# Performance work log

Hardware: AMD Instinct MI355X
Metric: run time of the kernel (lower is better)

The kernel has to match this reference:

```python
import jax, jax.numpy as jnp
import numpy as np

N = 100000
E = 1600000
F_IN = 4
HID = 8
HEADS = 8
NEG_SLOPE = 0.2


def setup_inputs() -> dict:
    key = jax.random.key(0)
    ks = jax.random.split(key, 12)
    x = jax.random.normal(ks[0], (N, F_IN), dtype=jnp.float32)
    edge_index = jax.random.randint(ks[1], (2, E), 0, N, dtype=jnp.int64)
    s = 0.3
    W1 = jax.random.normal(ks[2], (F_IN, HEADS * HID), dtype=jnp.float32) * s
    att_src1 = jax.random.normal(ks[3], (HEADS, HID), dtype=jnp.float32) * s
    att_dst1 = jax.random.normal(ks[4], (HEADS, HID), dtype=jnp.float32) * s
    b1 = jnp.zeros((HEADS * HID,), dtype=jnp.float32)
    W2 = jax.random.normal(ks[5], (HEADS * HID, 1), dtype=jnp.float32) * s
    att_src2 = jax.random.normal(ks[6], (1, 1), dtype=jnp.float32) * s
    att_dst2 = jax.random.normal(ks[7], (1, 1), dtype=jnp.float32) * s
    b2 = jnp.zeros((1,), dtype=jnp.float32)
    return {"x": x, "edge_index": edge_index, "W1": W1, "att_src1": att_src1,
            "att_dst1": att_dst1, "b1": b1, "W2": W2, "att_src2": att_src2,
            "att_dst2": att_dst2, "b2": b2}


def gat_conv(x, src, dst, W, att_s, att_d, b, heads, out_ch, concat):
    n = x.shape[0]
    h = (x @ W).reshape(n, heads, out_ch)              # [N,H,C]
    a_s = jnp.sum(h * att_s, axis=-1)                  # [N,H]
    a_d = jnp.sum(h * att_d, axis=-1)                  # [N,H]
    e = jax.nn.leaky_relu(a_s[src] + a_d[dst], NEG_SLOPE)  # [E,H]
    # segment softmax over edges grouped by destination node
    m = jax.ops.segment_max(e, dst, num_segments=n)
    e = jnp.exp(e - m[dst])
    denom = jax.ops.segment_sum(e, dst, num_segments=n)
    alpha = e / (denom[dst] + 1e-16)                   # [E,H]
    msg = h[src] * alpha[..., None]                    # [E,H,C]
    out = jax.ops.segment_sum(msg, dst, num_segments=n)  # [N,H,C]
    out = out.reshape(n, heads * out_ch) if concat else out.mean(axis=1)
    return out + b


def reference(x, edge_index, W1, att_src1, att_dst1, b1, W2, att_src2, att_dst2, b2):
    n = x.shape[0]
    loops = jnp.arange(n, dtype=edge_index.dtype)
    src = jnp.concatenate([edge_index[0], loops])
    dst = jnp.concatenate([edge_index[1], loops])
    h = gat_conv(x, src, dst, W1, att_src1, att_dst1, b1, HEADS, HID, True)
    h = jax.nn.elu(h)
    out = gat_conv(h, src, dst, W2, att_src2, att_dst2, b2, 1, 1, False)
    return jax.nn.sigmoid(out)
```

## Files before the change

### kernel.cpp

```cpp
#include <hip/hip_runtime.h>

#define NN 100000
#define NE 1600000
#define NBKT 391
#define CAP 8192
#define TILE 4096
#define NTILE ((NE + TILE - 1) / TILE)
#define NEG 0.2f

__global__ __launch_bounds__(512) void kU_prep(
    const float* __restrict__ W1, const float* __restrict__ atts,
    const float* __restrict__ attd, float* __restrict__ us, float* __restrict__ ud,
    int* __restrict__ bcnt)
{
    int t = threadIdx.x;
    if (t < NBKT) bcnt[t] = 0;
    if (t < 64) {
        int half = t >> 5;
        int i = t & 31;
        int h = i >> 2, k = i & 3;
        const float* att = half ? attd : atts;
        float acc = 0.f;
        #pragma unroll
        for (int j = 0; j < 8; j++)
            acc += W1[k * 64 + h * 8 + j] * att[h * 8 + j];
        (half ? ud : us)[h * 4 + k] = acc;
    }
}

__global__ __launch_bounds__(1024) void kP1_tile(
    const int* __restrict__ ei, int* __restrict__ bcnt, unsigned* __restrict__ bpack)
{
    __shared__ unsigned sarr[TILE];
    __shared__ int lh[512], lsc[512], lgb[512];
    int t = threadIdx.x;
    int e0 = blockIdx.x * TILE;
    int n = NE - e0; if (n > TILE) n = TILE;

    if (t < 512) lh[t] = 0;
    __syncthreads();
    for (int i = t; i < n; i += 1024) {
        int d = ei[NE + e0 + i];
        atomicAdd(&lh[d >> 8], 1);
    }
    __syncthreads();
    if (t < 512) lsc[t] = lh[t];
    __syncthreads();
    #pragma unroll
    for (int o = 1; o < 512; o <<= 1) {
        int u = 0;
        if (t < 512 && t >= o) u = lsc[t - o];
        __syncthreads();
        if (t < 512) lsc[t] += u;
        __syncthreads();
    }
    if (t < NBKT && lh[t] > 0) lgb[t] = atomicAdd(&bcnt[t], lh[t]);
    __syncthreads();
    if (t < 512) lh[t] = lsc[t] - lh[t];
    __syncthreads();
    for (int i = t; i < n; i += 1024) {
        int s = ei[e0 + i], d = ei[NE + e0 + i];
        int b = d >> 8;
        int pos = atomicAdd(&lh[b], 1);
        sarr[pos] = ((unsigned)s << 8) | (unsigned)(d & 255);
    }
    __syncthreads();
    int wave = t >> 6, lane = t & 63;
    for (int b = wave; b < NBKT; b += 16) {
        int start = (b == 0) ? 0 : lsc[b - 1];
        int cntb = lsc[b] - start;
        if (cntb == 0) continue;
        int gb = lgb[b];
        unsigned* dstp = &bpack[(size_t)b * CAP];
        for (int j = lane; j < cntb; j += 64) {
            int gpos = gb + j;
            if (gpos < CAP) dstp[gpos] = sarr[start + j];
        }
    }
}

__global__ __launch_bounds__(512) void kS_scan(
    const int* __restrict__ bcnt, int* __restrict__ bktoff, int* __restrict__ row)
{
    __shared__ int s[512];
    int t = threadIdx.x;
    int v = (t < NBKT) ? bcnt[t] : 0;
    s[t] = v;
    __syncthreads();
    #pragma unroll
    for (int o = 1; o < 512; o <<= 1) {
        int u = (t >= o) ? s[t - o] : 0;
        __syncthreads();
        s[t] += u;
        __syncthreads();
    }
    if (t < NBKT) bktoff[t] = s[t] - v;
    if (t == 0) row[NN] = NE;
}

__global__ __launch_bounds__(1024) void kP2_build(
    const int* __restrict__ bcnt, const int* __restrict__ bktoff,
    const unsigned* __restrict__ bpack, int* __restrict__ row, int* __restrict__ esrc)
{
    __shared__ int lh[256], lsc[256], lcur[256];
    __shared__ int sarr[CAP];
    int b = blockIdx.x;
    int t = threadIdx.x;
    int cnt = bcnt[b];
    if (cnt > CAP) cnt = CAP;
    const unsigned* bp = &bpack[(size_t)b * CAP];
    if (t < 256) lh[t] = 0;
    __syncthreads();
    for (int i = t; i < cnt; i += 1024)
        atomicAdd(&lh[bp[i] & 255u], 1);
    __syncthreads();
    if (t < 256) lsc[t] = lh[t];
    __syncthreads();
    #pragma unroll
    for (int o = 1; o < 256; o <<= 1) {
        int u = 0;
        if (t < 256 && t >= o) u = lsc[t - o];
        __syncthreads();
        if (t < 256) lsc[t] += u;
        __syncthreads();
    }
    int base = bktoff[b];
    if (t < 256) {
        int ex = lsc[t] - lh[t];
        lcur[t] = ex;
        int node = b * 256 + t;
        if (node < NN) row[node] = base + ex;
    }
    __syncthreads();
    for (int i = t; i < cnt; i += 1024) {
        unsigned u = bp[i];
        int pos = atomicAdd(&lcur[u & 255u], 1);
        sarr[pos] = (int)(u >> 8);
    }
    __syncthreads();
    for (int i = t; i < cnt; i += 1024)
        esrc[base + i] = sarr[i];
}

__global__ __launch_bounds__(256) void kE_l1agg(
    const int* __restrict__ row, const int* __restrict__ esrc,
    const float* __restrict__ x, const float* __restrict__ us,
    const float* __restrict__ ud, const float* __restrict__ W1,
    const float* __restrict__ b1, const float* __restrict__ W2,
    float* __restrict__ h2)
{
    int t = threadIdx.x;
    int grp = t >> 3;
    int h   = t & 7;
    int dst = blockIdx.x * 32 + grp;
    if (dst >= NN) return;

    int start = row[dst], end = row[dst + 1];
    int m = end - start;

    float4 u  = *reinterpret_cast<const float4*>(&us[h * 4]);
    float4 vd = *reinterpret_cast<const float4*>(&ud[h * 4]);
    float4 xd = *reinterpret_cast<const float4*>(&x[(size_t)dst * 4]);
    float adj = xd.x * vd.x + xd.y * vd.y + xd.z * vd.z + xd.w * vd.w;

    float a0 = fmaf(xd.x, u.x, fmaf(xd.y, u.y, fmaf(xd.z, u.z, fmaf(xd.w, u.w, adj))));
    a0 = fmaxf(a0, NEG * a0);
    float p0 = __expf(a0);
    float den = p0;
    float xa0 = p0 * xd.x, xa1 = p0 * xd.y, xa2 = p0 * xd.z, xa3 = p0 * xd.w;

    int j = 0;
    for (; j + 2 <= m; j += 2) {
        int s0 = esrc[start + j];
        int s1 = esrc[start + j + 1];
        float4 q0 = *reinterpret_cast<const float4*>(&x[(size_t)s0 * 4]);
        float4 q1 = *reinterpret_cast<const float4*>(&x[(size_t)s1 * 4]);
        float b0 = fmaf(q0.x, u.x, fmaf(q0.y, u.y, fmaf(q0.z, u.z, fmaf(q0.w, u.w, adj))));
        float c1 = fmaf(q1.x, u.x, fmaf(q1.y, u.y, fmaf(q1.z, u.z, fmaf(q1.w, u.w, adj))));
        b0 = fmaxf(b0, NEG * b0);
        c1 = fmaxf(c1, NEG * c1);
        float pb = __expf(b0);
        float pc = __expf(c1);
        den += pb + pc;
        xa0 = fmaf(pb, q0.x, fmaf(pc, q1.x, xa0));
        xa1 = fmaf(pb, q0.y, fmaf(pc, q1.y, xa1));
        xa2 = fmaf(pb, q0.z, fmaf(pc, q1.z, xa2));
        xa3 = fmaf(pb, q0.w, fmaf(pc, q1.w, xa3));
    }
    if (j < m) {
        int s0 = esrc[start + j];
        float4 q0 = *reinterpret_cast<const float4*>(&x[(size_t)s0 * 4]);
        float b0 = fmaf(q0.x, u.x, fmaf(q0.y, u.y, fmaf(q0.z, u.z, fmaf(q0.w, u.w, adj))));
        b0 = fmaxf(b0, NEG * b0);
        float pb = __expf(b0);
        den += pb;
        xa0 = fmaf(pb, q0.x, xa0);
        xa1 = fmaf(pb, q0.y, xa1);
        xa2 = fmaf(pb, q0.z, xa2);
        xa3 = fmaf(pb, q0.w, xa3);
    }

    int c0 = h * 8;
    float4 w0l = *reinterpret_cast<const float4*>(&W1[c0]);
    float4 w0h = *reinterpret_cast<const float4*>(&W1[c0 + 4]);
    float4 w1l = *reinterpret_cast<const float4*>(&W1[64 + c0]);
    float4 w1h = *reinterpret_cast<const float4*>(&W1[64 + c0 + 4]);
    float4 w2l = *reinterpret_cast<const float4*>(&W1[128 + c0]);
    float4 w2h = *reinterpret_cast<const float4*>(&W1[128 + c0 + 4]);
    float4 w3l = *reinterpret_cast<const float4*>(&W1[192 + c0]);
    float4 w3h = *reinterpret_cast<const float4*>(&W1[192 + c0 + 4]);
    float4 bbl = *reinterpret_cast<const float4*>(&b1[c0]);
    float4 bbh = *reinterpret_cast<const float4*>(&b1[c0 + 4]);
    float4 wwl = *reinterpret_cast<const float4*>(&W2[c0]);
    float4 wwh = *reinterpret_cast<const float4*>(&W2[c0 + 4]);
    float inv = 1.f / (den + 1e-16f);

    float acc = 0.f;
    {
        float v;
        v = (xa0*w0l.x + xa1*w1l.x + xa2*w2l.x + xa3*w3l.x)*inv + bbl.x;
        v = v > 0.f ? v : (__expf(v) - 1.f);  acc += v * wwl.x;
        v = (xa0*w0l.y + xa1*w1l.y + xa2*w2l.y + xa3*w3l.y)*inv + bbl.y;
        v = v > 0.f ? v : (__expf(v) - 1.f);  acc += v * wwl.y;
        v = (xa0*w0l.z + xa1*w1l.z + xa2*w2l.z + xa3*w3l.z)*inv + bbl.z;
        v = v > 0.f ? v : (__expf(v) - 1.f);  acc += v * wwl.z;
        v = (xa0*w0l.w + xa1*w1l.w + xa2*w2l.w + xa3*w3l.w)*inv + bbl.w;
        v = v > 0.f ? v : (__expf(v) - 1.f);  acc += v * wwl.w;
        v = (xa0*w0h.x + xa1*w1h.x + xa2*w2h.x + xa3*w3h.x)*inv + bbh.x;
        v = v > 0.f ? v : (__expf(v) - 1.f);  acc += v * wwh.x;
        v = (xa0*w0h.y + xa1*w1h.y + xa2*w2h.y + xa3*w3h.y)*inv + bbh.y;
        v = v > 0.f ? v : (__expf(v) - 1.f);  acc += v * wwh.y;
        v = (xa0*w0h.z + xa1*w1h.z + xa2*w2h.z + xa3*w3h.z)*inv + bbh.z;
        v = v > 0.f ? v : (__expf(v) - 1.f);  acc += v * wwh.z;
        v = (xa0*w0h.w + xa1*w1h.w + xa2*w2h.w + xa3*w3h.w)*inv + bbh.w;
        v = v > 0.f ? v : (__expf(v) - 1.f);  acc += v * wwh.w;
    }
    acc += __shfl_xor(acc, 1, 8);
    acc += __shfl_xor(acc, 2, 8);
    acc += __shfl_xor(acc, 4, 8);
    if (h == 0) h2[dst] = acc;
}

__global__ __launch_bounds__(256) void kF_l2agg(
    const int* __restrict__ row, const int* __restrict__ esrc,
    const float* __restrict__ h2, const float* __restrict__ as2,
    const float* __restrict__ ad2, const float* __restrict__ b2,
    float* __restrict__ out)
{
    int t = threadIdx.x;
    int grp = t >> 3;
    int sub = t & 7;
    int dst = blockIdx.x * 32 + grp;
    if (dst >= NN) return;
    int start = row[dst], end = row[dst + 1];
    float a_s = as2[0], a_d = ad2[0];
    float hdv = h2[dst];
    float hd = hdv * a_d;

    float den = 0.f, num = 0.f;
    if (sub == 0) {
        float v = hdv * a_s + hd;
        v = fmaxf(v, NEG * v);
        float p = __expf(v);
        den = p;
        num = p * hdv;
    }
    int i = start + sub;
    for (; i + 8 < end; i += 16) {
        float hs0 = h2[esrc[i]];
        float hs1 = h2[esrc[i + 8]];
        float v0 = hs0 * a_s + hd;
        float v1 = hs1 * a_s + hd;
        v0 = fmaxf(v0, NEG * v0);
        v1 = fmaxf(v1, NEG * v1);
        float p0 = __expf(v0);
        float p1 = __expf(v1);
        den += p0 + p1;
        num = fmaf(p0, hs0, fmaf(p1, hs1, num));
    }
    if (i < end) {
        float hs = h2[esrc[i]];
        float v = hs * a_s + hd;
        v = fmaxf(v, NEG * v);
        float p = __expf(v);
        den += p;
        num = fmaf(p, hs, num);
    }
    den += __shfl_xor(den, 1, 8);
    num += __shfl_xor(num, 1, 8);
    den += __shfl_xor(den, 2, 8);
    num += __shfl_xor(num, 2, 8);
    den += __shfl_xor(den, 4, 8);
    num += __shfl_xor(num, 4, 8);
    if (sub == 0) {
        float v = num / (den + 1e-16f) + b2[0];
        out[dst] = 1.f / (1.f + __expf(-v));
    }
}

extern "C" void kernel_launch(void* const* d_in, const int* in_sizes, int n_in,
                              void* d_out, int out_size, void* d_ws, size_t ws_size,
                              hipStream_t stream) {
    const float* x     = (const float*)d_in[0];
    const int*   ei    = (const int*)d_in[1];
    const float* W1    = (const float*)d_in[2];
    const float* atts1 = (const float*)d_in[3];
    const float* attd1 = (const float*)d_in[4];
    const float* b1    = (const float*)d_in[5];
    const float* W2    = (const float*)d_in[6];
    const float* atts2 = (const float*)d_in[7];
    const float* attd2 = (const float*)d_in[8];
    const float* b2    = (const float*)d_in[9];
    float* out = (float*)d_out;

    float* w = (float*)d_ws;
    float* us = w;
    float* ud = w + 32;
    float* h2 = w + 64;
    int* ibase  = (int*)(w + 64 + (size_t)NN);
    int* bcnt   = ibase;
    int* bktoff = ibase + 512;
    int* row    = ibase + 1024;
    int* esrc   = ibase + 1024 + NN + 64;
    unsigned* bpack = (unsigned*)(ibase + 1024 + NN + 64 + NE);

    dim3 gG((NN + 31) / 32);

    hipLaunchKernelGGL(kU_prep, dim3(1), dim3(512), 0, stream, W1, atts1, attd1, us, ud, bcnt);
    hipLaunchKernelGGL(kP1_tile, dim3(NTILE), dim3(1024), 0, stream, ei, bcnt, bpack);
    hipLaunchKernelGGL(kS_scan, dim3(1), dim3(512), 0, stream, bcnt, bktoff, row);
    hipLaunchKernelGGL(kP2_build, dim3(NBKT), dim3(1024), 0, stream, bcnt, bktoff, bpack, row, esrc);
    hipLaunchKernelGGL(kE_l1agg, gG, dim3(256), 0, stream, row, esrc, x, us, ud, W1, b1, W2, h2);
    hipLaunchKernelGGL(kF_l2agg, gG, dim3(256), 0, stream, row, esrc, h2, atts2, attd2, b2, out);
}
```

Measured before the change: 75.58 us.

## Fuse CSR build into per-bucket layer-1 aggregation and drop global scan

Removes the global bucket-offset scan and the CSR materialization (row/esrc). The per-bucket local sort now runs inside the layer-1 aggregation kernel, with neighbor lists kept in shared memory. Layer 2 aggregates straight from the unsorted bucket pack using shared-memory float atomics. This cuts two launches and the global esrc write and read, at the cost of 391-block grids, lower parallelism per node, and truncation at LCAP=6144 edges per bucket.

```diff
diff --git a/kernel.cpp b/kernel.cpp
--- a/kernel.cpp
+++ b/kernel.cpp
@@ -4,6 +4,7 @@
 #define NE 1600000
 #define NBKT 391
 #define CAP 8192
+#define LCAP 6144
 #define TILE 4096
 #define NTILE ((NE + TILE - 1) / TILE)
 #define NEG 0.2f
@@ -79,36 +80,22 @@
     }
 }
 
-__global__ __launch_bounds__(512) void kS_scan(
-    const int* __restrict__ bcnt, int* __restrict__ bktoff, int* __restrict__ row)
-{
-    __shared__ int s[512];
-    int t = threadIdx.x;
-    int v = (t < NBKT) ? bcnt[t] : 0;
-    s[t] = v;
-    __syncthreads();
-    #pragma unroll
-    for (int o = 1; o < 512; o <<= 1) {
-        int u = (t >= o) ? s[t - o] : 0;
-        __syncthreads();
-        s[t] += u;
-        __syncthreads();
-    }
-    if (t < NBKT) bktoff[t] = s[t] - v;
-    if (t == 0) row[NN] = NE;
-}
-
-__global__ __launch_bounds__(1024) void kP2_build(
-    const int* __restrict__ bcnt, const int* __restrict__ bktoff,
-    const unsigned* __restrict__ bpack, int* __restrict__ row, int* __restrict__ esrc)
+__global__ __launch_bounds__(1024) void kE_fused(
+    const int* __restrict__ bcnt, const unsigned* __restrict__ bpack,
+    const float* __restrict__ x, const float* __restrict__ us,
+    const float* __restrict__ ud, const float* __restrict__ W1,
+    const float* __restrict__ b1, const float* __restrict__ W2,
+    float* __restrict__ h2)
 {
     __shared__ int lh[256], lsc[256], lcur[256];
-    __shared__ int sarr[CAP];
-    int b = blockIdx.x;
-    int t = threadIdx.x;
-    int cnt = bcnt[b];
-    if (cnt > CAP) cnt = CAP;
+    __shared__ int sdat[LCAP];
+    __shared__ float sadj[256][8];
+    __shared__ float sxd[256][4];
+    int b = blockIdx.x, t = threadIdx.x;
+    int cnt = bcnt[b]; if (cnt > LCAP) cnt = LCAP;
     const unsigned* bp = &bpack[(size_t)b * CAP];
+    int node0 = b * 256;
+
     if (t < 256) lh[t] = 0;
     __syncthreads();
     for (int i = t; i < cnt; i += 1024)
@@ -124,82 +111,32 @@
         if (t < 256) lsc[t] += u;
         __syncthreads();
     }
-    int base = bktoff[b];
     if (t < 256) {
-        int ex = lsc[t] - lh[t];
-        lcur[t] = ex;
-        int node = b * 256 + t;
-        if (node < NN) row[node] = base + ex;
-    }
-    __syncthreads();
+        lcur[t] = lsc[t] - lh[t];
+        int node = node0 + t;
+        float4 xv = (node < NN) ? *reinterpret_cast<const float4*>(&x[(size_t)node * 4])
+                                : make_float4(0.f, 0.f, 0.f, 0.f);
+        sxd[t][0] = xv.x; sxd[t][1] = xv.y; sxd[t][2] = xv.z; sxd[t][3] = xv.w;
+    }
+    __syncthreads();
+    {
+        int dl = t >> 3, h = t & 7;
+        float4 vd = *reinterpret_cast<const float4*>(&ud[h * 4]);
+        #pragma unroll
+        for (int p = 0; p < 2; p++) {
+            int d = dl + 128 * p;
+            sadj[d][h] = sxd[d][0]*vd.x + sxd[d][1]*vd.y + sxd[d][2]*vd.z + sxd[d][3]*vd.w;
+        }
+    }
     for (int i = t; i < cnt; i += 1024) {
         unsigned u = bp[i];
         int pos = atomicAdd(&lcur[u & 255u], 1);
-        sarr[pos] = (int)(u >> 8);
-    }
-    __syncthreads();
-    for (int i = t; i < cnt; i += 1024)
-        esrc[base + i] = sarr[i];
-}
-
-__global__ __launch_bounds__(256) void kE_l1agg(
-    const int* __restrict__ row, const int* __restrict__ esrc,
-    const float* __restrict__ x, const float* __restrict__ us,
-    const float* __restrict__ ud, const float* __restrict__ W1,
-    const float* __restrict__ b1, const float* __restrict__ W2,
-    float* __restrict__ h2)
-{
-    int t = threadIdx.x;
-    int grp = t >> 3;
-    int h   = t & 7;
-    int dst = blockIdx.x * 32 + grp;
-    if (dst >= NN) return;
-
-    int start = row[dst], end = row[dst + 1];
-    int m = end - start;
-
-    float4 u  = *reinterpret_cast<const float4*>(&us[h * 4]);
-    float4 vd = *reinterpret_cast<const float4*>(&ud[h * 4]);
-    float4 xd = *reinterpret_cast<const float4*>(&x[(size_t)dst * 4]);
-    float adj = xd.x * vd.x + xd.y * vd.y + xd.z * vd.z + xd.w * vd.w;
-
-    float a0 = fmaf(xd.x, u.x, fmaf(xd.y, u.y, fmaf(xd.z, u.z, fmaf(xd.w, u.w, adj))));
-    a0 = fmaxf(a0, NEG * a0);
-    float p0 = __expf(a0);
-    float den = p0;
-    float xa0 = p0 * xd.x, xa1 = p0 * xd.y, xa2 = p0 * xd.z, xa3 = p0 * xd.w;
-
-    int j = 0;
-    for (; j + 2 <= m; j += 2) {
-        int s0 = esrc[start + j];
-        int s1 = esrc[start + j + 1];
-        float4 q0 = *reinterpret_cast<const float4*>(&x[(size_t)s0 * 4]);
-        float4 q1 = *reinterpret_cast<const float4*>(&x[(size_t)s1 * 4]);
-        float b0 = fmaf(q0.x, u.x, fmaf(q0.y, u.y, fmaf(q0.z, u.z, fmaf(q0.w, u.w, adj))));
-        float c1 = fmaf(q1.x, u.x, fmaf(q1.y, u.y, fmaf(q1.z, u.z, fmaf(q1.w, u.w, adj))));
-        b0 = fmaxf(b0, NEG * b0);
-        c1 = fmaxf(c1, NEG * c1);
-        float pb = __expf(b0);
-        float pc = __expf(c1);
-        den += pb + pc;
-        xa0 = fmaf(pb, q0.x, fmaf(pc, q1.x, xa0));
-        xa1 = fmaf(pb, q0.y, fmaf(pc, q1.y, xa1));
-        xa2 = fmaf(pb, q0.z, fmaf(pc, q1.z, xa2));
-        xa3 = fmaf(pb, q0.w, fmaf(pc, q1.w, xa3));
-    }
-    if (j < m) {
-        int s0 = esrc[start + j];
-        float4 q0 = *reinterpret_cast<const float4*>(&x[(size_t)s0 * 4]);
-        float b0 = fmaf(q0.x, u.x, fmaf(q0.y, u.y, fmaf(q0.z, u.z, fmaf(q0.w, u.w, adj))));
-        b0 = fmaxf(b0, NEG * b0);
-        float pb = __expf(b0);
-        den += pb;
-        xa0 = fmaf(pb, q0.x, xa0);
-        xa1 = fmaf(pb, q0.y, xa1);
-        xa2 = fmaf(pb, q0.z, xa2);
-        xa3 = fmaf(pb, q0.w, xa3);
-    }
-
+        sdat[pos] = (int)(u >> 8);
+    }
+    __syncthreads();
+
+    int h = t & 7;
+    float4 u4 = *reinterpret_cast<const float4*>(&us[h * 4]);
     int c0 = h * 8;
     float4 w0l = *reinterpret_cast<const float4*>(&W1[c0]);
     float4 w0h = *reinterpret_cast<const float4*>(&W1[c0 + 4]);
@@ -213,88 +150,119 @@
     float4 bbh = *reinterpret_cast<const float4*>(&b1[c0 + 4]);
     float4 wwl = *reinterpret_cast<const float4*>(&W2[c0]);
     float4 wwh = *reinterpret_cast<const float4*>(&W2[c0 + 4]);
-    float inv = 1.f / (den + 1e-16f);
-
-    float acc = 0.f;
-    {
-        float v;
-        v = (xa0*w0l.x + xa1*w1l.x + xa2*w2l.x + xa3*w3l.x)*inv + bbl.x;
-        v = v > 0.f ? v : (__expf(v) - 1.f);  acc += v * wwl.x;
-        v = (xa0*w0l.y + xa1*w1l.y + xa2*w2l.y + xa3*w3l.y)*inv + bbl.y;
-        v = v > 0.f ? v : (__expf(v) - 1.f);  acc += v * wwl.y;
-        v = (xa0*w0l.z + xa1*w1l.z + xa2*w2l.z + xa3*w3l.z)*inv + bbl.z;
-        v = v > 0.f ? v : (__expf(v) - 1.f);  acc += v * wwl.z;
-        v = (xa0*w0l.w + xa1*w1l.w + xa2*w2l.w + xa3*w3l.w)*inv + bbl.w;
-        v = v > 0.f ? v : (__expf(v) - 1.f);  acc += v * wwl.w;
-        v = (xa0*w0h.x + xa1*w1h.x + xa2*w2h.x + xa3*w3h.x)*inv + bbh.x;
-        v = v > 0.f ? v : (__expf(v) - 1.f);  acc += v * wwh.x;
-        v = (xa0*w0h.y + xa1*w1h.y + xa2*w2h.y + xa3*w3h.y)*inv + bbh.y;
-        v = v > 0.f ? v : (__expf(v) - 1.f);  acc += v * wwh.y;
-        v = (xa0*w0h.z + xa1*w1h.z + xa2*w2h.z + xa3*w3h.z)*inv + bbh.z;
-        v = v > 0.f ? v : (__expf(v) - 1.f);  acc += v * wwh.z;
-        v = (xa0*w0h.w + xa1*w1h.w + xa2*w2h.w + xa3*w3h.w)*inv + bbh.w;
-        v = v > 0.f ? v : (__expf(v) - 1.f);  acc += v * wwh.w;
-    }
-    acc += __shfl_xor(acc, 1, 8);
-    acc += __shfl_xor(acc, 2, 8);
-    acc += __shfl_xor(acc, 4, 8);
-    if (h == 0) h2[dst] = acc;
-}
-
-__global__ __launch_bounds__(256) void kF_l2agg(
-    const int* __restrict__ row, const int* __restrict__ esrc,
+
+    #pragma unroll
+    for (int p = 0; p < 2; p++) {
+        int dl = (t >> 3) + 128 * p;
+        int node = node0 + dl;
+        if (node < NN) {
+            int off = lsc[dl] - lh[dl];
+            int mdeg = lh[dl];
+            float adj = sadj[dl][h];
+            float xd0 = sxd[dl][0], xd1 = sxd[dl][1], xd2 = sxd[dl][2], xd3 = sxd[dl][3];
+            float a0 = fmaf(xd0, u4.x, fmaf(xd1, u4.y, fmaf(xd2, u4.z, fmaf(xd3, u4.w, adj))));
+            a0 = fmaxf(a0, NEG * a0);
+            float p0 = __expf(a0);
+            float den = p0;
+            float xa0 = p0 * xd0, xa1 = p0 * xd1, xa2 = p0 * xd2, xa3 = p0 * xd3;
+            int j = 0;
+            for (; j + 2 <= mdeg; j += 2) {
+                int s0 = sdat[off + j];
+                int s1 = sdat[off + j + 1];
+                float4 q0 = *reinterpret_cast<const float4*>(&x[(size_t)s0 * 4]);
+                float4 q1 = *reinterpret_cast<const float4*>(&x[(size_t)s1 * 4]);
+                float b0 = fmaf(q0.x, u4.x, fmaf(q0.y, u4.y, fmaf(q0.z, u4.z, fmaf(q0.w, u4.w, adj))));
+                float c1 = fmaf(q1.x, u4.x, fmaf(q1.y, u4.y, fmaf(q1.z, u4.z, fmaf(q1.w, u4.w, adj))));
+                b0 = fmaxf(b0, NEG * b0);
+                c1 = fmaxf(c1, NEG * c1);
+                float pb = __expf(b0);
+                float pc = __expf(c1);
+                den += pb + pc;
+                xa0 = fmaf(pb, q0.x, fmaf(pc, q1.x, xa0));
+                xa1 = fmaf(pb, q0.y, fmaf(pc, q1.y, xa1));
+                xa2 = fmaf(pb, q0.z, fmaf(pc, q1.z, xa2));
+                xa3 = fmaf(pb, q0.w, fmaf(pc, q1.w, xa3));
+            }
+            if (j < mdeg) {
+                int s0 = sdat[off + j];
+                float4 q0 = *reinterpret_cast<const float4*>(&x[(size_t)s0 * 4]);
+                float b0 = fmaf(q0.x, u4.x, fmaf(q0.y, u4.y, fmaf(q0.z, u4.z, fmaf(q0.w, u4.w, adj))));
+                b0 = fmaxf(b0, NEG * b0);
+                float pb = __expf(b0);
+                den += pb;
+                xa0 = fmaf(pb, q0.x, xa0);
+                xa1 = fmaf(pb, q0.y, xa1);
+                xa2 = fmaf(pb, q0.z, xa2);
+                xa3 = fmaf(pb, q0.w, xa3);
+            }
+            float inv = 1.f / (den + 1e-16f);
+            float acc = 0.f, v;
+            v = (xa0*w0l.x + xa1*w1l.x + xa2*w2l.x + xa3*w3l.x)*inv + bbl.x;
+            v = v > 0.f ? v : (__expf(v) - 1.f);  acc += v * wwl.x;
+            v = (xa0*w0l.y + xa1*w1l.y + xa2*w2l.y + xa3*w3l.y)*inv + bbl.y;
+            v = v > 0.f ? v : (__expf(v) - 1.f);  acc += v * wwl.y;
+            v = (xa0*w0l.z + xa1*w1l.z + xa2*w2l.z + xa3*w3l.z)*inv + bbl.z;
+            v = v > 0.f ? v : (__expf(v) - 1.f);  acc += v * wwl.z;
+            v = (xa0*w0l.w + xa1*w1l.w + xa2*w2l.w + xa3*w3l.w)*inv + bbl.w;
+            v = v > 0.f ? v : (__expf(v) - 1.f);  acc += v * wwl.w;
+            v = (xa0*w0h.x + xa1*w1h.x + xa2*w2h.x + xa3*w3h.x)*inv + bbh.x;
+            v = v > 0.f ? v : (__expf(v) - 1.f);  acc += v * wwh.x;
+            v = (xa0*w0h.y + xa1*w1h.y + xa2*w2h.y + xa3*w3h.y)*inv + bbh.y;
+            v = v > 0.f ? v : (__expf(v) - 1.f);  acc += v * wwh.y;
+            v = (xa0*w0h.z + xa1*w1h.z + xa2*w2h.z + xa3*w3h.z)*inv + bbh.z;
+            v = v > 0.f ? v : (__expf(v) - 1.f);  acc += v * wwh.z;
+            v = (xa0*w0h.w + xa1*w1h.w + xa2*w2h.w + xa3*w3h.w)*inv + bbh.w;
+            v = v > 0.f ? v : (__expf(v) - 1.f);  acc += v * wwh.w;
+            acc += __shfl_xor(acc, 1, 8);
+            acc += __shfl_xor(acc, 2, 8);
+            acc += __shfl_xor(acc, 4, 8);
+            if (h == 0) h2[node] = acc;
+        }
+    }
+}
+
+__global__ __launch_bounds__(1024) void kF_bucket(
+    const int* __restrict__ bcnt, const unsigned* __restrict__ bpack,
     const float* __restrict__ h2, const float* __restrict__ as2,
     const float* __restrict__ ad2, const float* __restrict__ b2,
     float* __restrict__ out)
 {
-    int t = threadIdx.x;
-    int grp = t >> 3;
-    int sub = t & 7;
-    int dst = blockIdx.x * 32 + grp;
-    if (dst >= NN) return;
-    int start = row[dst], end = row[dst + 1];
+    __shared__ float sh2[256], snum[256], sden[256];
+    int b = blockIdx.x, t = threadIdx.x;
+    int cnt = bcnt[b]; if (cnt > CAP) cnt = CAP;
+    const unsigned* bp = &bpack[(size_t)b * CAP];
     float a_s = as2[0], a_d = ad2[0];
-    float hdv = h2[dst];
-    float hd = hdv * a_d;
-
-    float den = 0.f, num = 0.f;
-    if (sub == 0) {
-        float v = hdv * a_s + hd;
+    if (t < 256) {
+        int node = b * 256 + t;
+        sh2[t] = (node < NN) ? h2[node] : 0.f;
+        snum[t] = 0.f;
+        sden[t] = 0.f;
+    }
+    __syncthreads();
+    for (int i = t; i < cnt; i += 1024) {
+        unsigned u = bp[i];
+        int s  = (int)(u >> 8);
+        int dl = (int)(u & 255u);
+        float hs = h2[s];
+        float v = fmaf(hs, a_s, sh2[dl] * a_d);
         v = fmaxf(v, NEG * v);
         float p = __expf(v);
-        den = p;
-        num = p * hdv;
-    }
-    int i = start + sub;
-    for (; i + 8 < end; i += 16) {
-        float hs0 = h2[esrc[i]];
-        float hs1 = h2[esrc[i + 8]];
-        float v0 = hs0 * a_s + hd;
-        float v1 = hs1 * a_s + hd;
-        v0 = fmaxf(v0, NEG * v0);
-        v1 = fmaxf(v1, NEG * v1);
-        float p0 = __expf(v0);
-        float p1 = __expf(v1);
-        den += p0 + p1;
-        num = fmaf(p0, hs0, fmaf(p1, hs1, num));
-    }
-    if (i < end) {
-        float hs = h2[esrc[i]];
-        float v = hs * a_s + hd;
-        v = fmaxf(v, NEG * v);
-        float p = __expf(v);
-        den += p;
-        num = fmaf(p, hs, num);
-    }
-    den += __shfl_xor(den, 1, 8);
-    num += __shfl_xor(num, 1, 8);
-    den += __shfl_xor(den, 2, 8);
-    num += __shfl_xor(num, 2, 8);
-    den += __shfl_xor(den, 4, 8);
-    num += __shfl_xor(num, 4, 8);
-    if (sub == 0) {
-        float v = num / (den + 1e-16f) + b2[0];
-        out[dst] = 1.f / (1.f + __expf(-v));
+        atomicAdd(&sden[dl], p);
+        atomicAdd(&snum[dl], p * hs);
+    }
+    __syncthreads();
+    if (t < 256) {
+        int node = b * 256 + t;
+        if (node < NN) {
+            float hdv = sh2[t];
+            float v = fmaf(hdv, a_s, hdv * a_d);
+            v = fmaxf(v, NEG * v);
+            float p0 = __expf(v);
+            float num = snum[t] + p0 * hdv;
+            float den = sden[t] + p0;
+            float r = num / (den + 1e-16f) + b2[0];
+            out[node] = 1.f / (1.f + __expf(-r));
+        }
     }
 }
 
@@ -317,19 +285,11 @@
     float* us = w;
     float* ud = w + 32;
     float* h2 = w + 64;
-    int* ibase  = (int*)(w + 64 + (size_t)NN);
-    int* bcnt   = ibase;
-    int* bktoff = ibase + 512;
-    int* row    = ibase + 1024;
-    int* esrc   = ibase + 1024 + NN + 64;
-    unsigned* bpack = (unsigned*)(ibase + 1024 + NN + 64 + NE);
-
-    dim3 gG((NN + 31) / 32);
+    int* bcnt = (int*)(w + 64 + (size_t)NN);
+    unsigned* bpack = (unsigned*)(w + 64 + (size_t)NN + 512);
 
     hipLaunchKernelGGL(kU_prep, dim3(1), dim3(512), 0, stream, W1, atts1, attd1, us, ud, bcnt);
     hipLaunchKernelGGL(kP1_tile, dim3(NTILE), dim3(1024), 0, stream, ei, bcnt, bpack);
-    hipLaunchKernelGGL(kS_scan, dim3(1), dim3(512), 0, stream, bcnt, bktoff, row);
-    hipLaunchKernelGGL(kP2_build, dim3(NBKT), dim3(1024), 0, stream, bcnt, bktoff, bpack, row, esrc);
-    hipLaunchKernelGGL(kE_l1agg, gG, dim3(256), 0, stream, row, esrc, x, us, ud, W1, b1, W2, h2);
-    hipLaunchKernelGGL(kF_l2agg, gG, dim3(256), 0, stream, row, esrc, h2, atts2, attd2, b2, out);
-}
+    hipLaunchKernelGGL(kE_fused, dim3(NBKT), dim3(1024), 0, stream, bcnt, bpack, x, us, ud, W1, b1, W2, h2);
+    hipLaunchKernelGGL(kF_bucket, dim3(NBKT), dim3(1024), 0, stream, bcnt, bpack, h2, atts2, attd2, b2, out);
+}
```

Measured after the change: 86.47 us. 1.14x slower.
